# Performance work log

Hardware: AMD Instinct MI355X
Metric: run time of the kernel (lower is better)

The kernel has to match this reference:

```python
import jax, jax.numpy as jnp
import numpy as np

TAG_SIZE = 50
START = TAG_SIZE - 2  # index of '<START>'
STOP = TAG_SIZE - 1   # index of '<STOP>'
B, S = 64, 512


def setup_inputs() -> dict:
    key = jax.random.key(0)
    k1, k2, k3 = jax.random.split(key, 3)
    feats = jax.random.normal(k1, (B, S, TAG_SIZE), dtype=jnp.float32)
    mask = jnp.ones((B, S), dtype=jnp.int32)
    tags = jax.random.randint(k2, (B, S), 0, START)  # valid tags exclude START/STOP
    transitions = jax.random.normal(k3, (TAG_SIZE, TAG_SIZE), dtype=jnp.float32)
    return {"feats": feats, "mask": mask, "tags": tags, "transitions": transitions}


def reference(feats, mask, tags, transitions):
    """CRF neg_log_likelihood_loss = forward_score (log partition, summed) - gold_score.
    feats: (B,S,T) emissions; mask: (B,S) {0,1}; tags: (B,S) gold tags;
    transitions[i,j] = score of transitioning from tag i to tag j.
    """
    b, s, t = feats.shape
    maskf = mask.astype(feats.dtype)

    # ---- forward algorithm (log partition) via scan over time ----
    feats_t = jnp.swapaxes(feats, 0, 1)            # (S,B,T)
    mask_t = jnp.swapaxes(mask, 0, 1).astype(bool)  # (S,B)
    # t=0: partition[b,j] = feats[b,0,j] + transitions[START, j]
    partition0 = feats_t[0] + transitions[START][None, :]  # (B,T)

    def step(partition, xs):
        f_t, m_t = xs  # (B,T), (B,)
        # cur_values[b,i,j] = partition[b,i] + transitions[i,j] + feats[b,t,j]
        cur_values = partition[:, :, None] + transitions[None, :, :] + f_t[:, None, :]
        cur = jax.nn.logsumexp(cur_values, axis=1)  # (B,T) logsumexp over prev tag
        new_partition = jnp.where(m_t[:, None], cur, partition)
        return new_partition, None

    partition, _ = jax.lax.scan(step, partition0, (feats_t[1:], mask_t[1:]))
    terminal = jax.nn.logsumexp(partition[:, :, None] + transitions[None, :, :], axis=1)  # (B,T)
    forward_score = terminal[:, STOP].sum()

    # ---- gold score ----
    # prev tag at step 0 is START, otherwise tags[:, t-1]
    prev = jnp.concatenate([jnp.full((b, 1), START, dtype=tags.dtype), tags[:, :-1]], axis=1)
    emit = jnp.take_along_axis(feats, tags[..., None], axis=2)[..., 0]  # (B,S)
    trans = transitions[prev, tags]                                      # (B,S)
    tg_energy = ((emit + trans) * maskf).sum()
    lengths = mask.astype(jnp.int32).sum(axis=1)                         # (B,)
    end_ids = jnp.take_along_axis(tags, (lengths - 1)[:, None].astype(tags.dtype), axis=1)[:, 0]
    end_energy = transitions[end_ids, STOP].sum()
    gold_score = tg_energy + end_energy

    return forward_score - gold_score
```

## Files before the change

### kernel.cpp

```cpp
#include <hip/hip_runtime.h>
#include <hip/hip_bf16.h>

#define T 50
#define NB 64
#define NS 512
#define START_TAG 48
#define STOP_TAG 49
#define NCH 8
#define CHL 64
#define PITCH 72

typedef _Float16 f16_t;
typedef _Float16 f16x2 __attribute__((ext_vector_type(2)));
typedef _Float16 f16x4 __attribute__((ext_vector_type(4)));
typedef _Float16 f16x8 __attribute__((ext_vector_type(8)));
typedef float    f32x4 __attribute__((ext_vector_type(4)));

static constexpr float LOG2E = 1.4426950408889634f;
static constexpr float LN2F  = 0.6931471805599453f;
static constexpr float S_E   = 6.0f;
#define NEG_BIG (-1.0e38f)

__device__ __forceinline__ float fexp2(float x) { return __builtin_amdgcn_exp2f(x); }
__device__ __forceinline__ float flog2(float x) { return __builtin_amdgcn_logf(x); }
__device__ __forceinline__ f16x2 bcast_h2(f16x2 v, int src) {
    unsigned u = __builtin_amdgcn_readlane(__builtin_bit_cast(unsigned, v), src);
    return __builtin_bit_cast(f16x2, u);
}
__device__ __forceinline__ f16x2 pack_h2(float a, float b) {
    return __builtin_bit_cast(f16x2, __builtin_amdgcn_cvt_pkrtz(a, b));
}

__device__ __forceinline__ float wave_fmax_dpp(float x) {
#define DPP_STEP(ctrl)                                                        \
    do {                                                                      \
        int _s = __builtin_bit_cast(int, x);                                  \
        int _p = __builtin_amdgcn_update_dpp(_s, _s, (ctrl), 0xf, 0xf, false);\
        x = fmaxf(x, __builtin_bit_cast(float, _p));                          \
    } while (0)
    DPP_STEP(0x111);
    DPP_STEP(0x112);
    DPP_STEP(0x114);
    DPP_STEP(0x118);
    DPP_STEP(0x142);
    DPP_STEP(0x143);
#undef DPP_STEP
    return __builtin_bit_cast(float,
        __builtin_amdgcn_readlane(__builtin_bit_cast(int, x), 63));
}

__global__ __launch_bounds__(256, 1)
void crf_chunk(const float* __restrict__ feats, const int* __restrict__ mask,
               const float* __restrict__ trans, f16_t* __restrict__ wsCt,
               float* __restrict__ wsD) {
    const int c    = blockIdx.x;
    const int b    = blockIdx.y;
    const int tid  = threadIdx.x;
    const int w    = tid >> 6;
    const int lane = tid & 63;
    const int l15  = lane & 15;
    const int q    = lane >> 4;

    __shared__ f16_t sC[64 * PITCH];
    __shared__ float sF[CHL][64];
    __shared__ int   sMk[CHL];

    const int t0  = c * CHL + 1;
    const int nst = NS - t0 < CHL ? NS - t0 : CHL;

    f16x8 Efrag[2][4];
    #pragma unroll
    for (int kb = 0; kb < 2; kb++)
        #pragma unroll
        for (int c2 = 0; c2 < 4; c2++) {
            f16x8 v;
            const int j = 4 * l15 + c2;
            #pragma unroll
            for (int jj = 0; jj < 8; jj++) {
                int kk = 32 * kb + q * 8 + jj;
                float x = 0.f;
                if (kk < T && j < T) x = fexp2(fmaf(trans[kk * T + j], LOG2E, -S_E));
                v[jj] = (f16_t)x;
            }
            Efrag[kb][c2] = v;
        }

    for (int r = w; r < CHL; r += 4) {
        int tl = t0 + r; tl = tl < NS ? tl : NS - 1;
        float fv = (lane < T && r < nst) ? feats[((size_t)b * NS + tl) * T + lane] : 0.f;
        sF[r][lane] = (lane < T && r < nst) ? fexp2(fv * LOG2E) : 0.f;
    }
    if (tid < CHL) {
        int tl = t0 + tid; tl = tl < NS ? tl : NS - 1;
        sMk[tid] = (tid < nst) ? mask[b * NS + tl] : 0;
    }

    for (int idx = tid; idx < 64 * PITCH; idx += 256) sC[idx] = (f16_t)0.f;
    if (tid < 64) sC[tid * PITCH + tid] = (f16_t)1.f;
    __syncthreads();

    float D   = 0.f;
    float mxw = 1.f;
    int   mk  = sMk[0];

    for (int s = 0; s < nst; s++) {
        const bool doit = (mk != 0);
        mk = (s + 1 < CHL) ? sMk[s + 1] : 0;

        if (doit) {
            int ebits = (int)((__float_as_uint(mxw) >> 23) & 255) - 127;
            ebits = ebits > 14 ? 14 : (ebits < -14 ? -14 : ebits);
            const float descale = __uint_as_float((unsigned)(127 - ebits) << 23);
            D += (float)ebits + S_E;

            const int abase = (16 * w + l15) * PITCH + 8 * q;
            f16x8 A0 = *(const f16x8*)&sC[abase];
            f16x8 A1 = *(const f16x8*)&sC[abase + 32];

            f32x4 acc[4];
            #pragma unroll
            for (int c2 = 0; c2 < 4; c2++) {
                acc[c2] = __builtin_amdgcn_mfma_f32_16x16x32_f16(A0, Efrag[0][c2],
                                                                 (f32x4){0.f,0.f,0.f,0.f}, 0, 0, 0);
                acc[c2] = __builtin_amdgcn_mfma_f32_16x16x32_f16(A1, Efrag[1][c2],
                                                                 acc[c2], 0, 0, 0);
            }

            f32x4 csv = *(const f32x4*)&sF[s][4 * l15];
            f32x4 cs2;
            #pragma unroll
            for (int c2 = 0; c2 < 4; c2++) cs2[c2] = csv[c2] * descale;

            float wmax = 0.f;
            #pragma unroll
            for (int r = 0; r < 4; r++) {
                f16x4 hv;
                #pragma unroll
                for (int c2 = 0; c2 < 4; c2++) {
                    float v = acc[c2][r] * cs2[c2];
                    wmax = fmaxf(wmax, v);
                    hv[c2] = (f16_t)v;
                }
                *(f16x4*)&sC[(16 * w + 4 * q + r) * PITCH + 4 * l15] = hv;
            }

            mxw = wave_fmax_dpp(wmax);
        }
    }

    __syncthreads();

    {
        const int col = tid >> 2;
        const int r0  = (tid & 3) << 4;
        unsigned short tmp[16];
        #pragma unroll
        for (int r = 0; r < 16; r++)
            tmp[r] = __builtin_bit_cast(unsigned short, sC[(r0 + r) * PITCH + col]);
        f16_t* dst = wsCt + ((size_t)(b * NCH + c)) * 4096 + col * 64 + r0;
        ((int4*)dst)[0] = *(const int4*)&tmp[0];
        ((int4*)dst)[1] = *(const int4*)&tmp[8];
    }
    if (lane == 0) wsD[(b * NCH + c) * 4 + w] = D;
}

__global__ __launch_bounds__(64, 1)
void crf_combine(const float* __restrict__ feats, const int* __restrict__ mask,
                 const int* __restrict__ tags, const float* __restrict__ trans,
                 const f16_t* __restrict__ wsCt, const float* __restrict__ wsD,
                 float* __restrict__ out) {
    const int b    = blockIdx.x;
    const int lane = threadIdx.x;

    float gsum = 0.f;
    int   lcnt = 0;
    for (int s = lane; s < NS; s += 64) {
        int   m  = mask[b * NS + s];
        int   tg = tags[b * NS + s];
        int   pv = (s == 0) ? START_TAG : tags[b * NS + s - 1];
        float e  = feats[((size_t)b * NS + s) * T + tg];
        float tr = trans[pv * T + tg];
        if (m) { gsum += e + tr; lcnt += 1; }
    }
    #pragma unroll
    for (int off = 32; off > 0; off >>= 1) {
        gsum += __shfl_down(gsum, off, 64);
        lcnt += __shfl_down(lcnt, off, 64);
    }
    float goldb = 0.f;
    if (lane == 0) goldb = gsum + trans[tags[b * NS + lcnt - 1] * T + STOP_TAG];

    float part = (lane < T)
        ? (feats[(size_t)b * NS * T + lane] + trans[START_TAG * T + lane]) * LOG2E
        : NEG_BIG;

    float Dq[NCH];
    #pragma unroll
    for (int c = 0; c < NCH; c++)
        Dq[c] = wsD[(b * NCH + c) * 4 + (lane >> 4)];

    int cur[32], nxt[32];
    {
        const f16_t* src = wsCt + (size_t)b * NCH * 4096 + lane * 64;
        #pragma unroll
        for (int kk = 0; kk < 8; kk++)
            *(int4*)&cur[4 * kk] = ((const int4*)src)[kk];
    }

    #pragma unroll
    for (int c = 0; c < NCH; c++) {
        if (c + 1 < NCH) {
            const f16_t* src = wsCt + (size_t)(b * NCH + c + 1) * 4096 + lane * 64;
            #pragma unroll
            for (int kk = 0; kk < 8; kk++)
                *(int4*)&nxt[4 * kk] = ((const int4*)src)[kk];
        }

        float tmp = part + Dq[c];
        float sft = wave_fmax_dpp(tmp);
        float ex  = fexp2(tmp - sft);
        float exo = __shfl_xor(ex, 1, 64);
        f16x2 pk  = pack_h2(ex, exo);

        float a0 = 0.f, a1 = 0.f, a2 = 0.f, a3 = 0.f;
        #pragma unroll
        for (int k = 0; k < 25; k += 4) {
            a0 = __builtin_amdgcn_fdot2(bcast_h2(pk, 2 * k), __builtin_bit_cast(f16x2, cur[k]), a0, false);
            if (k + 1 < 25) a1 = __builtin_amdgcn_fdot2(bcast_h2(pk, 2 * (k + 1)), __builtin_bit_cast(f16x2, cur[k + 1]), a1, false);
            if (k + 2 < 25) a2 = __builtin_amdgcn_fdot2(bcast_h2(pk, 2 * (k + 2)), __builtin_bit_cast(f16x2, cur[k + 2]), a2, false);
            if (k + 3 < 25) a3 = __builtin_amdgcn_fdot2(bcast_h2(pk, 2 * (k + 3)), __builtin_bit_cast(f16x2, cur[k + 3]), a3, false);
        }
        part = sft + flog2((a0 + a1) + (a2 + a3));

        if (c + 1 < NCH) {
            #pragma unroll
            for (int kk = 0; kk < 32; kk++) cur[kk] = nxt[kk];
        }
    }

    float v = (lane < T) ? part + trans[lane * T + STOP_TAG] * LOG2E : NEG_BIG;
    float mx = wave_fmax_dpp(v);
    float ee = (lane < T) ? fexp2(v - mx) : 0.f;
    #pragma unroll
    for (int off = 32; off > 0; off >>= 1) ee += __shfl_xor(ee, off, 64);
    if (lane == 0) {
        float fwd = (mx + flog2(ee)) * LN2F;
        atomicAdd(out, fwd - goldb);
    }
}

extern "C" void kernel_launch(void* const* d_in, const int* in_sizes, int n_in,
                              void* d_out, int out_size, void* d_ws, size_t ws_size,
                              hipStream_t stream) {
    const float* feats = (const float*)d_in[0];
    const int*   mask  = (const int*)d_in[1];
    const int*   tags  = (const int*)d_in[2];
    const float* trans = (const float*)d_in[3];
    float* out = (float*)d_out;

    f16_t* wsCt = (f16_t*)d_ws;
    float* wsD  = (float*)((char*)d_ws + (size_t)NB * NCH * 4096 * sizeof(f16_t));

    (void)hipMemsetAsync(out, 0, sizeof(float) * out_size, stream);
    crf_chunk<<<dim3(NCH, NB), 256, 0, stream>>>(feats, mask, trans, wsCt, wsD);
    crf_combine<<<NB, 64, 0, stream>>>(feats, mask, tags, trans, wsCt, wsD, out);
}
```

Measured before the change: 121.5 us.

## Split CRF scan into 16 shorter chunks and overlap gold score in combine

Templates the chunk kernel on chunk count and length, and launches 16 chunks of 32 steps per batch when workspace allows. This halves the serial per-block scan length and doubles the number of blocks, at the cost of doubling the chunk matrices the combine kernel must multiply serially. The combine kernel now runs the gold-score reduction on a second wave concurrently with the forward combine. The per-step mask is read from a ballot bitmask instead of shared memory, and address computations are hoisted out of the loop.

```diff
diff --git a/kernel.cpp b/kernel.cpp
--- a/kernel.cpp
+++ b/kernel.cpp
@@ -6,8 +6,6 @@
 #define NS 512
 #define START_TAG 48
 #define STOP_TAG 49
-#define NCH 8
-#define CHL 64
 #define PITCH 72
 
 typedef _Float16 f16_t;
@@ -49,6 +47,7 @@
         __builtin_amdgcn_readlane(__builtin_bit_cast(int, x), 63));
 }
 
+template<int NCHT, int CHLT>
 __global__ __launch_bounds__(256, 1)
 void crf_chunk(const float* __restrict__ feats, const int* __restrict__ mask,
                const float* __restrict__ trans, f16_t* __restrict__ wsCt,
@@ -62,11 +61,10 @@
     const int q    = lane >> 4;
 
     __shared__ f16_t sC[64 * PITCH];
-    __shared__ float sF[CHL][64];
-    __shared__ int   sMk[CHL];
-
-    const int t0  = c * CHL + 1;
-    const int nst = NS - t0 < CHL ? NS - t0 : CHL;
+    __shared__ float sF[CHLT][64];
+
+    const int t0  = c * CHLT + 1;
+    const int nst = NS - t0 < CHLT ? NS - t0 : CHLT;
 
     f16x8 Efrag[2][4];
     #pragma unroll
@@ -85,14 +83,17 @@
             Efrag[kb][c2] = v;
         }
 
-    for (int r = w; r < CHL; r += 4) {
+    for (int r = w; r < CHLT; r += 4) {
         int tl = t0 + r; tl = tl < NS ? tl : NS - 1;
         float fv = (lane < T && r < nst) ? feats[((size_t)b * NS + tl) * T + lane] : 0.f;
         sF[r][lane] = (lane < T && r < nst) ? fexp2(fv * LOG2E) : 0.f;
     }
-    if (tid < CHL) {
-        int tl = t0 + tid; tl = tl < NS ? tl : NS - 1;
-        sMk[tid] = (tid < nst) ? mask[b * NS + tl] : 0;
+
+    unsigned long long bm;
+    {
+        int tl = t0 + lane; tl = tl < NS ? tl : NS - 1;
+        int mv = (lane < nst) ? mask[b * NS + tl] : 0;
+        bm = __ballot(mv != 0);
     }
 
     for (int idx = tid; idx < 64 * PITCH; idx += 256) sC[idx] = (f16_t)0.f;
@@ -101,21 +102,19 @@
 
     float D   = 0.f;
     float mxw = 1.f;
-    int   mk  = sMk[0];
+    const int abase  = (16 * w + l15) * PITCH + 8 * q;
+    const int sbase0 = (16 * w + 4 * q) * PITCH + 4 * l15;
 
     for (int s = 0; s < nst; s++) {
-        const bool doit = (mk != 0);
-        mk = (s + 1 < CHL) ? sMk[s + 1] : 0;
-
-        if (doit) {
+        if ((bm >> s) & 1ull) {
             int ebits = (int)((__float_as_uint(mxw) >> 23) & 255) - 127;
             ebits = ebits > 14 ? 14 : (ebits < -14 ? -14 : ebits);
             const float descale = __uint_as_float((unsigned)(127 - ebits) << 23);
             D += (float)ebits + S_E;
 
-            const int abase = (16 * w + l15) * PITCH + 8 * q;
-            f16x8 A0 = *(const f16x8*)&sC[abase];
-            f16x8 A1 = *(const f16x8*)&sC[abase + 32];
+            f32x4 csv = *(const f32x4*)&sF[s][4 * l15];
+            f16x8 A0  = *(const f16x8*)&sC[abase];
+            f16x8 A1  = *(const f16x8*)&sC[abase + 32];
 
             f32x4 acc[4];
             #pragma unroll
@@ -126,7 +125,6 @@
                                                                  acc[c2], 0, 0, 0);
             }
 
-            f32x4 csv = *(const f32x4*)&sF[s][4 * l15];
             f32x4 cs2;
             #pragma unroll
             for (int c2 = 0; c2 < 4; c2++) cs2[c2] = csv[c2] * descale;
@@ -141,7 +139,7 @@
                     wmax = fmaxf(wmax, v);
                     hv[c2] = (f16_t)v;
                 }
-                *(f16x4*)&sC[(16 * w + 4 * q + r) * PITCH + 4 * l15] = hv;
+                *(f16x4*)&sC[sbase0 + r * PITCH] = hv;
             }
 
             mxw = wave_fmax_dpp(wmax);
@@ -157,96 +155,103 @@
         #pragma unroll
         for (int r = 0; r < 16; r++)
             tmp[r] = __builtin_bit_cast(unsigned short, sC[(r0 + r) * PITCH + col]);
-        f16_t* dst = wsCt + ((size_t)(b * NCH + c)) * 4096 + col * 64 + r0;
+        f16_t* dst = wsCt + ((size_t)(b * NCHT + c)) * 4096 + col * 64 + r0;
         ((int4*)dst)[0] = *(const int4*)&tmp[0];
         ((int4*)dst)[1] = *(const int4*)&tmp[8];
     }
-    if (lane == 0) wsD[(b * NCH + c) * 4 + w] = D;
-}
-
-__global__ __launch_bounds__(64, 1)
+    if (lane == 0) wsD[(b * NCHT + c) * 4 + w] = D;
+}
+
+template<int NCHT>
+__global__ __launch_bounds__(128, 1)
 void crf_combine(const float* __restrict__ feats, const int* __restrict__ mask,
                  const int* __restrict__ tags, const float* __restrict__ trans,
                  const f16_t* __restrict__ wsCt, const float* __restrict__ wsD,
                  float* __restrict__ out) {
     const int b    = blockIdx.x;
-    const int lane = threadIdx.x;
-
-    float gsum = 0.f;
-    int   lcnt = 0;
-    for (int s = lane; s < NS; s += 64) {
-        int   m  = mask[b * NS + s];
-        int   tg = tags[b * NS + s];
-        int   pv = (s == 0) ? START_TAG : tags[b * NS + s - 1];
-        float e  = feats[((size_t)b * NS + s) * T + tg];
-        float tr = trans[pv * T + tg];
-        if (m) { gsum += e + tr; lcnt += 1; }
-    }
-    #pragma unroll
-    for (int off = 32; off > 0; off >>= 1) {
-        gsum += __shfl_down(gsum, off, 64);
-        lcnt += __shfl_down(lcnt, off, 64);
-    }
-    float goldb = 0.f;
-    if (lane == 0) goldb = gsum + trans[tags[b * NS + lcnt - 1] * T + STOP_TAG];
-
-    float part = (lane < T)
-        ? (feats[(size_t)b * NS * T + lane] + trans[START_TAG * T + lane]) * LOG2E
-        : NEG_BIG;
-
-    float Dq[NCH];
-    #pragma unroll
-    for (int c = 0; c < NCH; c++)
-        Dq[c] = wsD[(b * NCH + c) * 4 + (lane >> 4)];
-
-    int cur[32], nxt[32];
-    {
-        const f16_t* src = wsCt + (size_t)b * NCH * 4096 + lane * 64;
-        #pragma unroll
-        for (int kk = 0; kk < 8; kk++)
-            *(int4*)&cur[4 * kk] = ((const int4*)src)[kk];
-    }
-
-    #pragma unroll
-    for (int c = 0; c < NCH; c++) {
-        if (c + 1 < NCH) {
-            const f16_t* src = wsCt + (size_t)(b * NCH + c + 1) * 4096 + lane * 64;
+    const int tid  = threadIdx.x;
+    const int wv   = tid >> 6;
+    const int lane = tid & 63;
+
+    __shared__ float sGold;
+    float fwd = 0.f;
+
+    if (wv == 1) {
+        float gsum = 0.f;
+        int   lcnt = 0;
+        for (int s = lane; s < NS; s += 64) {
+            int   m  = mask[b * NS + s];
+            int   tg = tags[b * NS + s];
+            int   pv = (s == 0) ? START_TAG : tags[b * NS + s - 1];
+            float e  = feats[((size_t)b * NS + s) * T + tg];
+            float tr = trans[pv * T + tg];
+            if (m) { gsum += e + tr; lcnt += 1; }
+        }
+        #pragma unroll
+        for (int off = 32; off > 0; off >>= 1) {
+            gsum += __shfl_down(gsum, off, 64);
+            lcnt += __shfl_down(lcnt, off, 64);
+        }
+        if (lane == 0) sGold = gsum + trans[tags[b * NS + lcnt - 1] * T + STOP_TAG];
+    } else {
+        float part = (lane < T)
+            ? (feats[(size_t)b * NS * T + lane] + trans[START_TAG * T + lane]) * LOG2E
+            : NEG_BIG;
+
+        float Dq[NCHT];
+        #pragma unroll
+        for (int c = 0; c < NCHT; c++)
+            Dq[c] = wsD[(b * NCHT + c) * 4 + (lane >> 4)];
+
+        int cur[32], nxt[32];
+        {
+            const f16_t* src = wsCt + (size_t)b * NCHT * 4096 + lane * 64;
             #pragma unroll
             for (int kk = 0; kk < 8; kk++)
-                *(int4*)&nxt[4 * kk] = ((const int4*)src)[kk];
-        }
-
-        float tmp = part + Dq[c];
-        float sft = wave_fmax_dpp(tmp);
-        float ex  = fexp2(tmp - sft);
-        float exo = __shfl_xor(ex, 1, 64);
-        f16x2 pk  = pack_h2(ex, exo);
-
-        float a0 = 0.f, a1 = 0.f, a2 = 0.f, a3 = 0.f;
-        #pragma unroll
-        for (int k = 0; k < 25; k += 4) {
-            a0 = __builtin_amdgcn_fdot2(bcast_h2(pk, 2 * k), __builtin_bit_cast(f16x2, cur[k]), a0, false);
-            if (k + 1 < 25) a1 = __builtin_amdgcn_fdot2(bcast_h2(pk, 2 * (k + 1)), __builtin_bit_cast(f16x2, cur[k + 1]), a1, false);
-            if (k + 2 < 25) a2 = __builtin_amdgcn_fdot2(bcast_h2(pk, 2 * (k + 2)), __builtin_bit_cast(f16x2, cur[k + 2]), a2, false);
-            if (k + 3 < 25) a3 = __builtin_amdgcn_fdot2(bcast_h2(pk, 2 * (k + 3)), __builtin_bit_cast(f16x2, cur[k + 3]), a3, false);
-        }
-        part = sft + flog2((a0 + a1) + (a2 + a3));
-
-        if (c + 1 < NCH) {
-            #pragma unroll
-            for (int kk = 0; kk < 32; kk++) cur[kk] = nxt[kk];
-        }
-    }
-
-    float v = (lane < T) ? part + trans[lane * T + STOP_TAG] * LOG2E : NEG_BIG;
-    float mx = wave_fmax_dpp(v);
-    float ee = (lane < T) ? fexp2(v - mx) : 0.f;
-    #pragma unroll
-    for (int off = 32; off > 0; off >>= 1) ee += __shfl_xor(ee, off, 64);
-    if (lane == 0) {
-        float fwd = (mx + flog2(ee)) * LN2F;
-        atomicAdd(out, fwd - goldb);
-    }
+                *(int4*)&cur[4 * kk] = ((const int4*)src)[kk];
+        }
+
+        #pragma unroll
+        for (int c = 0; c < NCHT; c++) {
+            if (c + 1 < NCHT) {
+                const f16_t* src = wsCt + (size_t)(b * NCHT + c + 1) * 4096 + lane * 64;
+                #pragma unroll
+                for (int kk = 0; kk < 8; kk++)
+                    *(int4*)&nxt[4 * kk] = ((const int4*)src)[kk];
+            }
+
+            float tmp = part + Dq[c];
+            float sft = wave_fmax_dpp(tmp);
+            float ex  = fexp2(tmp - sft);
+            float exo = __shfl_xor(ex, 1, 64);
+            f16x2 pk  = pack_h2(ex, exo);
+
+            float a0 = 0.f, a1 = 0.f, a2 = 0.f, a3 = 0.f;
+            #pragma unroll
+            for (int k = 0; k < 25; k += 4) {
+                a0 = __builtin_amdgcn_fdot2(bcast_h2(pk, 2 * k), __builtin_bit_cast(f16x2, cur[k]), a0, false);
+                if (k + 1 < 25) a1 = __builtin_amdgcn_fdot2(bcast_h2(pk, 2 * (k + 1)), __builtin_bit_cast(f16x2, cur[k + 1]), a1, false);
+                if (k + 2 < 25) a2 = __builtin_amdgcn_fdot2(bcast_h2(pk, 2 * (k + 2)), __builtin_bit_cast(f16x2, cur[k + 2]), a2, false);
+                if (k + 3 < 25) a3 = __builtin_amdgcn_fdot2(bcast_h2(pk, 2 * (k + 3)), __builtin_bit_cast(f16x2, cur[k + 3]), a3, false);
+            }
+            part = sft + flog2((a0 + a1) + (a2 + a3));
+
+            if (c + 1 < NCHT) {
+                #pragma unroll
+                for (int kk = 0; kk < 32; kk++) cur[kk] = nxt[kk];
+            }
+        }
+
+        float v = (lane < T) ? part + trans[lane * T + STOP_TAG] * LOG2E : NEG_BIG;
+        float mx = wave_fmax_dpp(v);
+        float ee = (lane < T) ? fexp2(v - mx) : 0.f;
+        #pragma unroll
+        for (int off = 32; off > 0; off >>= 1) ee += __shfl_xor(ee, off, 64);
+        fwd = (mx + flog2(ee)) * LN2F;
+    }
+
+    __syncthreads();
+    if (tid == 0) atomicAdd(out, fwd - sGold);
 }
 
 extern "C" void kernel_launch(void* const* d_in, const int* in_sizes, int n_in,
@@ -258,10 +263,21 @@
     const float* trans = (const float*)d_in[3];
     float* out = (float*)d_out;
 
-    f16_t* wsCt = (f16_t*)d_ws;
-    float* wsD  = (float*)((char*)d_ws + (size_t)NB * NCH * 4096 * sizeof(f16_t));
-
     (void)hipMemsetAsync(out, 0, sizeof(float) * out_size, stream);
-    crf_chunk<<<dim3(NCH, NB), 256, 0, stream>>>(feats, mask, trans, wsCt, wsD);
-    crf_combine<<<NB, 64, 0, stream>>>(feats, mask, tags, trans, wsCt, wsD, out);
-}
+
+    const size_t matBytes16 = (size_t)NB * 16 * 4096 * sizeof(f16_t);
+    const size_t need16     = matBytes16 + (size_t)NB * 16 * 4 * sizeof(float);
+
+    if (ws_size >= need16) {
+        f16_t* wsCt = (f16_t*)d_ws;
+        float* wsD  = (float*)((char*)d_ws + matBytes16);
+        crf_chunk<16, 32><<<dim3(16, NB), 256, 0, stream>>>(feats, mask, trans, wsCt, wsD);
+        crf_combine<16><<<NB, 128, 0, stream>>>(feats, mask, tags, trans, wsCt, wsD, out);
+    } else {
+        const size_t matBytes8 = (size_t)NB * 8 * 4096 * sizeof(f16_t);
+        f16_t* wsCt = (f16_t*)d_ws;
+        float* wsD  = (float*)((char*)d_ws + matBytes8);
+        crf_chunk<8, 64><<<dim3(8, NB), 256, 0, stream>>>(feats, mask, trans, wsCt, wsD);
+        crf_combine<8><<<NB, 128, 0, stream>>>(feats, mask, tags, trans, wsCt, wsD, out);
+    }
+}
```

New measurement: 117.8 us. 1.03x faster.
